# Kernel optimization log

Measured on AMD Instinct MI355X. Metric: run time of the kernel, lower is better.

The kernel has to match this reference:

```python
import jax, jax.numpy as jnp
import numpy as np
from jax import lax

DEPTH = 3
KS = 5

def haar_fwd(x):
    # x: (B, 2h, 2w, C) -> (B, h, w, C, 4) with bands [LL, LH, HL, HH]
    a = x[:, 0::2, 0::2]; b = x[:, 0::2, 1::2]
    c = x[:, 1::2, 0::2]; d = x[:, 1::2, 1::2]
    ll = (a + b + c + d) * 0.5
    lh = (a + b - c - d) * 0.5
    hl = (a - b + c - d) * 0.5
    hh = (a - b - c + d) * 0.5
    return jnp.stack([ll, lh, hl, hh], axis=-1)

def haar_inv(co):
    # co: (B, h, w, C, 4) -> (B, 2h, 2w, C); orthonormal inverse of haar_fwd
    ll, lh, hl, hh = co[..., 0], co[..., 1], co[..., 2], co[..., 3]
    a = (ll + lh + hl + hh) * 0.5
    b = (ll + lh - hl - hh) * 0.5
    c = (ll - lh + hl - hh) * 0.5
    d = (ll - lh - hl + hh) * 0.5
    B, h, w, C = ll.shape
    top = jnp.stack([a, b], axis=3).reshape(B, h, 2 * w, C)
    bot = jnp.stack([c, d], axis=3).reshape(B, h, 2 * w, C)
    return jnp.stack([top, bot], axis=2).reshape(B, 2 * h, 2 * w, C)

def depthwise(x, k, groups):
    return lax.conv_general_dilated(
        x, k, (1, 1), 'SAME',
        dimension_numbers=('NHWC', 'HWIO', 'NHWC'),
        feature_group_count=groups)

def setup_inputs() -> dict:
    key = jax.random.key(0)
    ks = jax.random.split(key, 2 + DEPTH)
    B, H, W, C = 8, 256, 256, 128
    x = jax.random.normal(ks[0], (B, H, W, C), jnp.float32)
    fan = float(KS * KS)
    base_kernel = jax.random.normal(ks[1], (KS, KS, 1, C), jnp.float32) / np.sqrt(fan)
    base_bias = jnp.zeros((C,), jnp.float32)
    base_scale = jnp.ones((1, 1, 1, C), jnp.float32)
    wavelet_kernels = tuple(
        jax.random.normal(ks[2 + i], (KS, KS, 1, C * 4), jnp.float32) / np.sqrt(fan)
        for i in range(DEPTH))
    wavelet_scales = tuple(jnp.full((1, 1, 1, C * 4), 0.1, jnp.float32) for _ in range(DEPTH))
    return dict(x=x, base_kernel=base_kernel, base_bias=base_bias, base_scale=base_scale,
                wavelet_kernels=wavelet_kernels, wavelet_scales=wavelet_scales)

def reference(x, base_kernel, base_bias, base_scale, wavelet_kernels, wavelet_scales):
    B, H, W, C = x.shape
    # pad input to even H/W (edge mode); no-op for even dims
    xp = jnp.pad(x, ((0, 0), (0, H % 2), (0, W % 2), (0, 0)), mode='edge')
    # multi-level Haar forward: level l decomposes the raw LL of level l-1
    coeffs, dims = [], []
    cur = xp
    for _ in range(DEPTH):
        _, h, w, _ = cur.shape
        dims.append((h, w))
        cur = jnp.pad(cur, ((0, 0), (0, h % 2), (0, w % 2), (0, 0)), mode='edge')
        co = haar_fwd(cur)
        coeffs.append(co)
        cur = co[..., 0]
    # per-level depthwise conv with scale fused into the kernel
    conv_coeffs = []
    for lvl in range(DEPTH):
        co = coeffs[lvl]
        Bc, h, w, Cc, _ = co.shape
        flat = co.reshape(Bc, h, w, Cc * 4)
        fused = wavelet_scales[lvl] * wavelet_kernels[lvl]  # (KS,KS,1,4C)
        out = depthwise(flat, fused, Cc * 4)
        conv_coeffs.append(out.reshape(Bc, h, w, Cc, 4))
    # inverse reconstruction with add of deeper reconstruction into LL band
    next_ll = jnp.zeros_like(conv_coeffs[-1][..., 0])
    for lvl in range(DEPTH - 1, -1, -1):
        co = conv_coeffs[lvl].at[..., 0].add(next_ll)
        rec = haar_inv(co)
        h, w = dims[lvl]
        next_ll = rec[:, :h, :w, :]
    output_wt = next_ll[:, :H, :W, :]
    x_base = base_scale * (depthwise(xp, base_kernel, C) + base_bias)[:, :H, :W, :]
    return x_base + output_wt
```

## Files before the change

### kernel.cpp

```cpp
#include <hip/hip_runtime.h>

#define NC 128
#define NB 8
#define CPB 32
#define R 2
#define JT 32

__device__ __forceinline__ float2 ld2(const float* p) { return *(const float2*)p; }
__device__ __forceinline__ float2 add2(float2 a, float2 b) { return make_float2(a.x + b.x, a.y + b.y); }
__device__ __forceinline__ float2 sub2(float2 a, float2 b) { return make_float2(a.x - b.x, a.y - b.y); }
__device__ __forceinline__ float2 muls2(float2 a, float s) { return make_float2(a.x * s, a.y * s); }
__device__ __forceinline__ float2 fma2(float2 a, float2 w, float2 c) {
    return make_float2(fmaf(a.x, w.x, c.x), fmaf(a.y, w.y, c.y));
}

__global__ __launch_bounds__(256) void k_haar_ll(
    const float* __restrict__ P, float* __restrict__ out, int h, int w)
{
    int idx = blockIdx.x * blockDim.x + threadIdx.x;
    int total = NB * h * w * (NC / 4);
    if (idx >= total) return;
    int cq = idx & (NC / 4 - 1);
    int t  = idx / (NC / 4);
    int j  = t % w; t /= w;
    int i  = t % h;
    int b  = t / h;
    size_t W2C  = (size_t)(2 * w) * NC;
    size_t base = (((size_t)b * (2 * h) + 2 * i) * (2 * w) + 2 * j) * NC + cq * 4;
    float4 A  = *(const float4*)(P + base);
    float4 Bv = *(const float4*)(P + base + NC);
    float4 Cv = *(const float4*)(P + base + W2C);
    float4 Dv = *(const float4*)(P + base + W2C + NC);
    float4 r;
    r.x = (A.x + Bv.x + Cv.x + Dv.x) * 0.5f;
    r.y = (A.y + Bv.y + Cv.y + Dv.y) * 0.5f;
    r.z = (A.z + Bv.z + Cv.z + Dv.z) * 0.5f;
    r.w = (A.w + Bv.w + Cv.w + Dv.w) * 0.5f;
    *(float4*)(out + (size_t)idx * 4) = r;
}

#define WL2(s, t)  (wl + ((s) * 25 + (t)) * CPB + 2 * tc)
#define WB2(m, n)  (wbase + ((m) * 5 + (n)) * CPB + 2 * tc)

template <bool BASE>
__global__ __launch_bounds__(256) void k_convinv(
    const float* __restrict__ P, const float* __restrict__ nll,
    const float* __restrict__ wk, const float* __restrict__ wsc,
    const float* __restrict__ bk, const float* __restrict__ bb,
    const float* __restrict__ bs, float* __restrict__ out,
    int h, int w)
{
    extern __shared__ float lds[];
    float* wl     = lds;
    float* wbase  = wl + 4 * 25 * CPB;
    float* bscale = wbase + 25 * CPB;
    float* bbias  = bscale + CPB;

    const int cg    = blockIdx.x & 3;
    const int jtile = blockIdx.x >> 2;
    const int c0    = cg * CPB;
    const int tid   = threadIdx.x + threadIdx.y * 16;

    for (int u = tid; u < 4 * 25 * CPB; u += 256) {
        int tcc = u & (CPB - 1);
        int st  = u / CPB;
        int t   = st % 25;
        int s   = st / 25;
        wl[u] = 0.5f * wsc[(c0 + tcc) * 4 + s] * wk[t * (4 * NC) + (c0 + tcc) * 4 + s];
    }
    if (BASE) {
        for (int u = tid; u < 25 * CPB; u += 256) {
            int tcc = u & (CPB - 1);
            int t   = u / CPB;
            wbase[u] = bk[t * NC + c0 + tcc];
        }
        if (tid < CPB) { bscale[tid] = bs[c0 + tid]; bbias[tid] = bb[c0 + tid]; }
    }
    __syncthreads();

    const int tc = threadIdx.x;
    const int cc = c0 + 2 * tc;
    const int b  = blockIdx.z;
    const int i  = blockIdx.y;
    const int ja = jtile * JT + threadIdx.y * R;
    const int PH = 2 * h;
    const size_t rowC = (size_t)(2 * w) * NC;

    int   coff[R + 4];
    float cmask[R + 4];
    #pragma unroll
    for (int q = 0; q < R + 4; ++q) {
        int xq  = ja + q - 2;
        int xqc = min(max(xq, 0), w - 1);
        coff[q]  = xqc * (2 * NC);
        cmask[q] = (xq >= 0 && xq < w) ? 1.f : 0.f;
    }

    float2 acc0[R], acc1[R], acc2[R], acc3[R];
    float2 bb00[R], bb01[R], bb10[R], bb11[R];
    #pragma unroll
    for (int s = 0; s < R; ++s) {
        acc0[s] = acc1[s] = acc2[s] = acc3[s] = make_float2(0.f, 0.f);
        bb00[s] = bb01[s] = bb10[s] = bb11[s] = make_float2(0.f, 0.f);
    }

    #pragma unroll
    for (int ky = 0; ky < 5; ++ky) {
        int y = i + ky - 2;
        if (y < 0 || y >= h) continue;

        const float* prA = P + ((size_t)b * PH + 2 * y) * rowC + cc;
        const float* prC = prA + rowC;
        #pragma unroll
        for (int q = 0; q < R + 4; ++q) {
            float m = cmask[q];
            const float* pA = prA + coff[q];
            const float* pC = prC + coff[q];
            float2 A  = muls2(ld2(pA), m);
            float2 Bv = muls2(ld2(pA + NC), m);
            float2 Cv = muls2(ld2(pC), m);
            float2 Dv = muls2(ld2(pC + NC), m);
            float2 sA = add2(A, Bv), sC = add2(Cv, Dv);
            float2 dA = sub2(A, Bv), dC = sub2(Cv, Dv);
            float2 s0 = add2(sA, sC), s1 = sub2(sA, sC);
            float2 s2 = add2(dA, dC), s3 = sub2(dA, dC);
            #pragma unroll
            for (int s = 0; s < R; ++s) {
                const int kx = q - s;
                if (kx < 0 || kx > 4) continue;
                const int t = ky * 5 + kx;
                acc0[s] = fma2(s0, ld2(WL2(0, t)), acc0[s]);
                acc1[s] = fma2(s1, ld2(WL2(1, t)), acc1[s]);
                acc2[s] = fma2(s2, ld2(WL2(2, t)), acc2[s]);
                acc3[s] = fma2(s3, ld2(WL2(3, t)), acc3[s]);
                if (BASE && ky >= 1 && ky <= 3 && kx >= 1 && kx <= 3) {
                    bb00[s] = fma2(A, ld2(WB2(2 * ky - 2, 2 * kx - 2)), bb00[s]);
                    if (kx >= 2)            bb01[s] = fma2(A,  ld2(WB2(2 * ky - 2, 2 * kx - 3)), bb01[s]);
                    if (ky >= 2)            bb10[s] = fma2(A,  ld2(WB2(2 * ky - 3, 2 * kx - 2)), bb10[s]);
                    if (ky >= 2 && kx >= 2) bb11[s] = fma2(A,  ld2(WB2(2 * ky - 3, 2 * kx - 3)), bb11[s]);
                    if (kx <= 2)            bb00[s] = fma2(Bv, ld2(WB2(2 * ky - 2, 2 * kx - 1)), bb00[s]);
                                            bb01[s] = fma2(Bv, ld2(WB2(2 * ky - 2, 2 * kx - 2)), bb01[s]);
                    if (ky >= 2 && kx <= 2) bb10[s] = fma2(Bv, ld2(WB2(2 * ky - 3, 2 * kx - 1)), bb10[s]);
                    if (ky >= 2)            bb11[s] = fma2(Bv, ld2(WB2(2 * ky - 3, 2 * kx - 2)), bb11[s]);
                    if (ky <= 2)            bb00[s] = fma2(Cv, ld2(WB2(2 * ky - 1, 2 * kx - 2)), bb00[s]);
                    if (ky <= 2 && kx >= 2) bb01[s] = fma2(Cv, ld2(WB2(2 * ky - 1, 2 * kx - 3)), bb01[s]);
                                            bb10[s] = fma2(Cv, ld2(WB2(2 * ky - 2, 2 * kx - 2)), bb10[s]);
                    if (kx >= 2)            bb11[s] = fma2(Cv, ld2(WB2(2 * ky - 2, 2 * kx - 3)), bb11[s]);
                    if (ky <= 2 && kx <= 2) bb00[s] = fma2(Dv, ld2(WB2(2 * ky - 1, 2 * kx - 1)), bb00[s]);
                    if (ky <= 2)            bb01[s] = fma2(Dv, ld2(WB2(2 * ky - 1, 2 * kx - 2)), bb01[s]);
                    if (kx <= 2)            bb10[s] = fma2(Dv, ld2(WB2(2 * ky - 2, 2 * kx - 1)), bb10[s]);
                                            bb11[s] = fma2(Dv, ld2(WB2(2 * ky - 2, 2 * kx - 2)), bb11[s]);
                }
            }
        }
    }

    #pragma unroll
    for (int s = 0; s < R; ++s) {
        int j = ja + s;
        float2 a0 = acc0[s];
        if (nll) a0 = add2(a0, ld2(nll + (((size_t)b * h + i) * w + j) * NC + cc));
        float2 av = muls2(add2(add2(a0, acc1[s]), add2(acc2[s], acc3[s])), 0.5f);
        float2 bv = muls2(sub2(add2(a0, acc1[s]), add2(acc2[s], acc3[s])), 0.5f);
        float2 cv = muls2(add2(sub2(a0, acc1[s]), sub2(acc2[s], acc3[s])), 0.5f);
        float2 dv = muls2(sub2(sub2(a0, acc1[s]), sub2(acc2[s], acc3[s])), 0.5f);

        size_t ob = ((size_t)b * PH + 2 * i) * rowC + (size_t)(2 * j) * NC + cc;
        if (BASE) {
            float2 sc = ld2(bscale + 2 * tc);
            float2 bi = ld2(bbias + 2 * tc);
            float2 o00 = add2(make_float2(sc.x * (bb00[s].x + bi.x), sc.y * (bb00[s].y + bi.y)), av);
            float2 o01 = add2(make_float2(sc.x * (bb01[s].x + bi.x), sc.y * (bb01[s].y + bi.y)), bv);
            float2 o10 = add2(make_float2(sc.x * (bb10[s].x + bi.x), sc.y * (bb10[s].y + bi.y)), cv);
            float2 o11 = add2(make_float2(sc.x * (bb11[s].x + bi.x), sc.y * (bb11[s].y + bi.y)), dv);
            *(float2*)(out + ob)             = o00;
            *(float2*)(out + ob + NC)        = o01;
            *(float2*)(out + ob + rowC)      = o10;
            *(float2*)(out + ob + rowC + NC) = o11;
        } else {
            *(float2*)(out + ob)             = av;
            *(float2*)(out + ob + NC)        = bv;
            *(float2*)(out + ob + rowC)      = cv;
            *(float2*)(out + ob + rowC + NC) = dv;
        }
    }
}

extern "C" void kernel_launch(void* const* d_in, const int* in_sizes, int n_in,
                              void* d_out, int out_size, void* d_ws, size_t ws_size,
                              hipStream_t stream)
{
    const float* x  = (const float*)d_in[0];
    const float* bk = (const float*)d_in[1];
    const float* bb = (const float*)d_in[2];
    const float* bs = (const float*)d_in[3];
    const float* wk[3];
    const float* wv[3];
    if (n_in >= 10) {
        for (int i = 0; i < 3; ++i) {
            wk[i] = (const float*)d_in[4 + i];
            wv[i] = (const float*)d_in[7 + i];
        }
    } else {
        const float* wkc = (const float*)d_in[4];
        const float* wvc = (const float*)d_in[5];
        for (int i = 0; i < 3; ++i) {
            wk[i] = wkc + (size_t)i * 25 * 4 * NC;
            wv[i] = wvc + (size_t)i * 4 * NC;
        }
    }
    float* out = (float*)d_out;

    float* ll0 = out;
    float* ll1 = out + 16777216;
    float* r2  = out + 16777216 + 4194304;
    float* r1  = (float*)d_ws;

    {
        int total = NB * 128 * 128 * (NC / 4);
        k_haar_ll<<<(total + 255) / 256, 256, 0, stream>>>(x, ll0, 128, 128);
    }
    {
        int total = NB * 64 * 64 * (NC / 4);
        k_haar_ll<<<(total + 255) / 256, 256, 0, stream>>>(ll0, ll1, 64, 64);
    }

    size_t lds_nb = (size_t)(4 * 25 * CPB) * sizeof(float);
    size_t lds_b  = (size_t)(4 * 25 * CPB + 25 * CPB + 2 * CPB) * sizeof(float);
    dim3 blk(16, 16);

    k_convinv<false><<<dim3((32 / JT) * 4, 32, NB), blk, lds_nb, stream>>>(
        ll1, nullptr, wk[2], wv[2], nullptr, nullptr, nullptr, r2, 32, 32);

    k_convinv<false><<<dim3((64 / JT) * 4, 64, NB), blk, lds_nb, stream>>>(
        ll0, r2, wk[1], wv[1], nullptr, nullptr, nullptr, r1, 64, 64);

    k_convinv<true><<<dim3((128 / JT) * 4, 128, NB), blk, lds_b, stream>>>(
        x, r1, wk[0], wv[0], bk, bb, bs, out, 128, 128);
}
```

Baseline: 646.3 us.

## Raise per-thread column blocking to 4 and split interior/boundary conv paths

Each thread now computes 4 output columns instead of 2, so it reuses more of the loaded input columns across outputs (R+4 loads for R outputs). The clamped-offset and mask arithmetic is dropped from an unmasked interior path, and edge threads take a separate per-output path with explicit bounds checks. Launch bounds now request 2 blocks per CU, and out-of-range threads return early for levels whose width is smaller than the tile. The cost is higher register pressure, since the BASE variant keeps 32 float2 accumulators, plus idle threads on the 32-wide level and divergence between interior and edge threads.

```diff
diff --git a/kernel.cpp b/kernel.cpp
--- a/kernel.cpp
+++ b/kernel.cpp
@@ -3,8 +3,8 @@
 #define NC 128
 #define NB 8
 #define CPB 32
-#define R 2
-#define JT 32
+#define R 4
+#define JT (16 * R)
 
 __device__ __forceinline__ float2 ld2(const float* p) { return *(const float2*)p; }
 __device__ __forceinline__ float2 add2(float2 a, float2 b) { return make_float2(a.x + b.x, a.y + b.y); }
@@ -43,7 +43,7 @@
 #define WB2(m, n)  (wbase + ((m) * 5 + (n)) * CPB + 2 * tc)
 
 template <bool BASE>
-__global__ __launch_bounds__(256) void k_convinv(
+__global__ __launch_bounds__(256, 2) void k_convinv(
     const float* __restrict__ P, const float* __restrict__ nll,
     const float* __restrict__ wk, const float* __restrict__ wsc,
     const float* __restrict__ bk, const float* __restrict__ bb,
@@ -83,18 +83,9 @@
     const int b  = blockIdx.z;
     const int i  = blockIdx.y;
     const int ja = jtile * JT + threadIdx.y * R;
+    if (ja >= w) return;
     const int PH = 2 * h;
     const size_t rowC = (size_t)(2 * w) * NC;
-
-    int   coff[R + 4];
-    float cmask[R + 4];
-    #pragma unroll
-    for (int q = 0; q < R + 4; ++q) {
-        int xq  = ja + q - 2;
-        int xqc = min(max(xq, 0), w - 1);
-        coff[q]  = xqc * (2 * NC);
-        cmask[q] = (xq >= 0 && xq < w) ? 1.f : 0.f;
-    }
 
     float2 acc0[R], acc1[R], acc2[R], acc3[R];
     float2 bb00[R], bb01[R], bb10[R], bb11[R];
@@ -104,52 +95,103 @@
         bb00[s] = bb01[s] = bb10[s] = bb11[s] = make_float2(0.f, 0.f);
     }
 
-    #pragma unroll
-    for (int ky = 0; ky < 5; ++ky) {
-        int y = i + ky - 2;
-        if (y < 0 || y >= h) continue;
-
-        const float* prA = P + ((size_t)b * PH + 2 * y) * rowC + cc;
-        const float* prC = prA + rowC;
+    const bool interior = (ja >= 2) && (ja <= w - R - 2);
+
+    if (interior) {
         #pragma unroll
-        for (int q = 0; q < R + 4; ++q) {
-            float m = cmask[q];
-            const float* pA = prA + coff[q];
-            const float* pC = prC + coff[q];
-            float2 A  = muls2(ld2(pA), m);
-            float2 Bv = muls2(ld2(pA + NC), m);
-            float2 Cv = muls2(ld2(pC), m);
-            float2 Dv = muls2(ld2(pC + NC), m);
-            float2 sA = add2(A, Bv), sC = add2(Cv, Dv);
-            float2 dA = sub2(A, Bv), dC = sub2(Cv, Dv);
-            float2 s0 = add2(sA, sC), s1 = sub2(sA, sC);
-            float2 s2 = add2(dA, dC), s3 = sub2(dA, dC);
+        for (int ky = 0; ky < 5; ++ky) {
+            int y = i + ky - 2;
+            if (y < 0 || y >= h) continue;
+
+            const float* pA0 = P + ((size_t)b * PH + 2 * y) * rowC
+                                 + (size_t)(ja - 2) * (2 * NC) + cc;
+            const float* pC0 = pA0 + rowC;
             #pragma unroll
-            for (int s = 0; s < R; ++s) {
-                const int kx = q - s;
-                if (kx < 0 || kx > 4) continue;
-                const int t = ky * 5 + kx;
-                acc0[s] = fma2(s0, ld2(WL2(0, t)), acc0[s]);
-                acc1[s] = fma2(s1, ld2(WL2(1, t)), acc1[s]);
-                acc2[s] = fma2(s2, ld2(WL2(2, t)), acc2[s]);
-                acc3[s] = fma2(s3, ld2(WL2(3, t)), acc3[s]);
-                if (BASE && ky >= 1 && ky <= 3 && kx >= 1 && kx <= 3) {
-                    bb00[s] = fma2(A, ld2(WB2(2 * ky - 2, 2 * kx - 2)), bb00[s]);
-                    if (kx >= 2)            bb01[s] = fma2(A,  ld2(WB2(2 * ky - 2, 2 * kx - 3)), bb01[s]);
-                    if (ky >= 2)            bb10[s] = fma2(A,  ld2(WB2(2 * ky - 3, 2 * kx - 2)), bb10[s]);
-                    if (ky >= 2 && kx >= 2) bb11[s] = fma2(A,  ld2(WB2(2 * ky - 3, 2 * kx - 3)), bb11[s]);
-                    if (kx <= 2)            bb00[s] = fma2(Bv, ld2(WB2(2 * ky - 2, 2 * kx - 1)), bb00[s]);
-                                            bb01[s] = fma2(Bv, ld2(WB2(2 * ky - 2, 2 * kx - 2)), bb01[s]);
-                    if (ky >= 2 && kx <= 2) bb10[s] = fma2(Bv, ld2(WB2(2 * ky - 3, 2 * kx - 1)), bb10[s]);
-                    if (ky >= 2)            bb11[s] = fma2(Bv, ld2(WB2(2 * ky - 3, 2 * kx - 2)), bb11[s]);
-                    if (ky <= 2)            bb00[s] = fma2(Cv, ld2(WB2(2 * ky - 1, 2 * kx - 2)), bb00[s]);
-                    if (ky <= 2 && kx >= 2) bb01[s] = fma2(Cv, ld2(WB2(2 * ky - 1, 2 * kx - 3)), bb01[s]);
-                                            bb10[s] = fma2(Cv, ld2(WB2(2 * ky - 2, 2 * kx - 2)), bb10[s]);
-                    if (kx >= 2)            bb11[s] = fma2(Cv, ld2(WB2(2 * ky - 2, 2 * kx - 3)), bb11[s]);
-                    if (ky <= 2 && kx <= 2) bb00[s] = fma2(Dv, ld2(WB2(2 * ky - 1, 2 * kx - 1)), bb00[s]);
-                    if (ky <= 2)            bb01[s] = fma2(Dv, ld2(WB2(2 * ky - 1, 2 * kx - 2)), bb01[s]);
-                    if (kx <= 2)            bb10[s] = fma2(Dv, ld2(WB2(2 * ky - 2, 2 * kx - 1)), bb10[s]);
-                                            bb11[s] = fma2(Dv, ld2(WB2(2 * ky - 2, 2 * kx - 2)), bb11[s]);
+            for (int q = 0; q < R + 4; ++q) {
+                float2 A  = ld2(pA0 + q * 2 * NC);
+                float2 Bv = ld2(pA0 + q * 2 * NC + NC);
+                float2 Cv = ld2(pC0 + q * 2 * NC);
+                float2 Dv = ld2(pC0 + q * 2 * NC + NC);
+                float2 sA = add2(A, Bv), sC = add2(Cv, Dv);
+                float2 dA = sub2(A, Bv), dC = sub2(Cv, Dv);
+                float2 s0 = add2(sA, sC), s1 = sub2(sA, sC);
+                float2 s2 = add2(dA, dC), s3 = sub2(dA, dC);
+                #pragma unroll
+                for (int s = 0; s < R; ++s) {
+                    const int kx = q - s;
+                    if (kx < 0 || kx > 4) continue;
+                    const int t = ky * 5 + kx;
+                    acc0[s] = fma2(s0, ld2(WL2(0, t)), acc0[s]);
+                    acc1[s] = fma2(s1, ld2(WL2(1, t)), acc1[s]);
+                    acc2[s] = fma2(s2, ld2(WL2(2, t)), acc2[s]);
+                    acc3[s] = fma2(s3, ld2(WL2(3, t)), acc3[s]);
+                    if (BASE && ky >= 1 && ky <= 3 && kx >= 1 && kx <= 3) {
+                        bb00[s] = fma2(A, ld2(WB2(2 * ky - 2, 2 * kx - 2)), bb00[s]);
+                        if (kx >= 2)            bb01[s] = fma2(A,  ld2(WB2(2 * ky - 2, 2 * kx - 3)), bb01[s]);
+                        if (ky >= 2)            bb10[s] = fma2(A,  ld2(WB2(2 * ky - 3, 2 * kx - 2)), bb10[s]);
+                        if (ky >= 2 && kx >= 2) bb11[s] = fma2(A,  ld2(WB2(2 * ky - 3, 2 * kx - 3)), bb11[s]);
+                        if (kx <= 2)            bb00[s] = fma2(Bv, ld2(WB2(2 * ky - 2, 2 * kx - 1)), bb00[s]);
+                                                bb01[s] = fma2(Bv, ld2(WB2(2 * ky - 2, 2 * kx - 2)), bb01[s]);
+                        if (ky >= 2 && kx <= 2) bb10[s] = fma2(Bv, ld2(WB2(2 * ky - 3, 2 * kx - 1)), bb10[s]);
+                        if (ky >= 2)            bb11[s] = fma2(Bv, ld2(WB2(2 * ky - 3, 2 * kx - 2)), bb11[s]);
+                        if (ky <= 2)            bb00[s] = fma2(Cv, ld2(WB2(2 * ky - 1, 2 * kx - 2)), bb00[s]);
+                        if (ky <= 2 && kx >= 2) bb01[s] = fma2(Cv, ld2(WB2(2 * ky - 1, 2 * kx - 3)), bb01[s]);
+                                                bb10[s] = fma2(Cv, ld2(WB2(2 * ky - 2, 2 * kx - 2)), bb10[s]);
+                        if (kx >= 2)            bb11[s] = fma2(Cv, ld2(WB2(2 * ky - 2, 2 * kx - 3)), bb11[s]);
+                        if (ky <= 2 && kx <= 2) bb00[s] = fma2(Dv, ld2(WB2(2 * ky - 1, 2 * kx - 1)), bb00[s]);
+                        if (ky <= 2)            bb01[s] = fma2(Dv, ld2(WB2(2 * ky - 1, 2 * kx - 2)), bb01[s]);
+                        if (kx <= 2)            bb10[s] = fma2(Dv, ld2(WB2(2 * ky - 2, 2 * kx - 1)), bb10[s]);
+                                                bb11[s] = fma2(Dv, ld2(WB2(2 * ky - 2, 2 * kx - 2)), bb11[s]);
+                    }
+                }
+            }
+        }
+    } else {
+        #pragma unroll
+        for (int s = 0; s < R; ++s) {
+            int j = ja + s;
+            if (j >= w) break;
+            #pragma unroll
+            for (int ky = 0; ky < 5; ++ky) {
+                int y = i + ky - 2;
+                if (y < 0 || y >= h) continue;
+                const float* prA = P + ((size_t)b * PH + 2 * y) * rowC + cc;
+                const float* prC = prA + rowC;
+                #pragma unroll
+                for (int kx = 0; kx < 5; ++kx) {
+                    int xq = j + kx - 2;
+                    if (xq < 0 || xq >= w) continue;
+                    const float* pA = prA + (size_t)xq * (2 * NC);
+                    const float* pC = prC + (size_t)xq * (2 * NC);
+                    float2 A  = ld2(pA);
+                    float2 Bv = ld2(pA + NC);
+                    float2 Cv = ld2(pC);
+                    float2 Dv = ld2(pC + NC);
+                    float2 sA = add2(A, Bv), sC = add2(Cv, Dv);
+                    float2 dA = sub2(A, Bv), dC = sub2(Cv, Dv);
+                    const int t = ky * 5 + kx;
+                    acc0[s] = fma2(add2(sA, sC), ld2(WL2(0, t)), acc0[s]);
+                    acc1[s] = fma2(sub2(sA, sC), ld2(WL2(1, t)), acc1[s]);
+                    acc2[s] = fma2(add2(dA, dC), ld2(WL2(2, t)), acc2[s]);
+                    acc3[s] = fma2(sub2(dA, dC), ld2(WL2(3, t)), acc3[s]);
+                    if (BASE && ky >= 1 && ky <= 3 && kx >= 1 && kx <= 3) {
+                        bb00[s] = fma2(A, ld2(WB2(2 * ky - 2, 2 * kx - 2)), bb00[s]);
+                        if (kx >= 2)            bb01[s] = fma2(A,  ld2(WB2(2 * ky - 2, 2 * kx - 3)), bb01[s]);
+                        if (ky >= 2)            bb10[s] = fma2(A,  ld2(WB2(2 * ky - 3, 2 * kx - 2)), bb10[s]);
+                        if (ky >= 2 && kx >= 2) bb11[s] = fma2(A,  ld2(WB2(2 * ky - 3, 2 * kx - 3)), bb11[s]);
+                        if (kx <= 2)            bb00[s] = fma2(Bv, ld2(WB2(2 * ky - 2, 2 * kx - 1)), bb00[s]);
+                                                bb01[s] = fma2(Bv, ld2(WB2(2 * ky - 2, 2 * kx - 2)), bb01[s]);
+                        if (ky >= 2 && kx <= 2) bb10[s] = fma2(Bv, ld2(WB2(2 * ky - 3, 2 * kx - 1)), bb10[s]);
+                        if (ky >= 2)            bb11[s] = fma2(Bv, ld2(WB2(2 * ky - 3, 2 * kx - 2)), bb11[s]);
+                        if (ky <= 2)            bb00[s] = fma2(Cv, ld2(WB2(2 * ky - 1, 2 * kx - 2)), bb00[s]);
+                        if (ky <= 2 && kx >= 2) bb01[s] = fma2(Cv, ld2(WB2(2 * ky - 1, 2 * kx - 3)), bb01[s]);
+                                                bb10[s] = fma2(Cv, ld2(WB2(2 * ky - 2, 2 * kx - 2)), bb10[s]);
+                        if (kx >= 2)            bb11[s] = fma2(Cv, ld2(WB2(2 * ky - 2, 2 * kx - 3)), bb11[s]);
+                        if (ky <= 2 && kx <= 2) bb00[s] = fma2(Dv, ld2(WB2(2 * ky - 1, 2 * kx - 1)), bb00[s]);
+                        if (ky <= 2)            bb01[s] = fma2(Dv, ld2(WB2(2 * ky - 1, 2 * kx - 2)), bb01[s]);
+                        if (kx <= 2)            bb10[s] = fma2(Dv, ld2(WB2(2 * ky - 2, 2 * kx - 1)), bb10[s]);
+                                                bb11[s] = fma2(Dv, ld2(WB2(2 * ky - 2, 2 * kx - 2)), bb11[s]);
+                    }
                 }
             }
         }
@@ -158,6 +200,7 @@
     #pragma unroll
     for (int s = 0; s < R; ++s) {
         int j = ja + s;
+        if (j >= w) break;
         float2 a0 = acc0[s];
         if (nll) a0 = add2(a0, ld2(nll + (((size_t)b * h + i) * w + j) * NC + cc));
         float2 av = muls2(add2(add2(a0, acc1[s]), add2(acc2[s], acc3[s])), 0.5f);
@@ -169,14 +212,10 @@
         if (BASE) {
             float2 sc = ld2(bscale + 2 * tc);
             float2 bi = ld2(bbias + 2 * tc);
-            float2 o00 = add2(make_float2(sc.x * (bb00[s].x + bi.x), sc.y * (bb00[s].y + bi.y)), av);
-            float2 o01 = add2(make_float2(sc.x * (bb01[s].x + bi.x), sc.y * (bb01[s].y + bi.y)), bv);
-            float2 o10 = add2(make_float2(sc.x * (bb10[s].x + bi.x), sc.y * (bb10[s].y + bi.y)), cv);
-            float2 o11 = add2(make_float2(sc.x * (bb11[s].x + bi.x), sc.y * (bb11[s].y + bi.y)), dv);
-            *(float2*)(out + ob)             = o00;
-            *(float2*)(out + ob + NC)        = o01;
-            *(float2*)(out + ob + rowC)      = o10;
-            *(float2*)(out + ob + rowC + NC) = o11;
+            *(float2*)(out + ob)             = add2(make_float2(sc.x * (bb00[s].x + bi.x), sc.y * (bb00[s].y + bi.y)), av);
+            *(float2*)(out + ob + NC)        = add2(make_float2(sc.x * (bb01[s].x + bi.x), sc.y * (bb01[s].y + bi.y)), bv);
+            *(float2*)(out + ob + rowC)      = add2(make_float2(sc.x * (bb10[s].x + bi.x), sc.y * (bb10[s].y + bi.y)), cv);
+            *(float2*)(out + ob + rowC + NC) = add2(make_float2(sc.x * (bb11[s].x + bi.x), sc.y * (bb11[s].y + bi.y)), dv);
         } else {
             *(float2*)(out + ob)             = av;
             *(float2*)(out + ob + NC)        = bv;
@@ -229,12 +268,12 @@
     size_t lds_b  = (size_t)(4 * 25 * CPB + 25 * CPB + 2 * CPB) * sizeof(float);
     dim3 blk(16, 16);
 
-    k_convinv<false><<<dim3((32 / JT) * 4, 32, NB), blk, lds_nb, stream>>>(
+    k_convinv<false><<<dim3(((32 + JT - 1) / JT) * 4, 32, NB), blk, lds_nb, stream>>>(
         ll1, nullptr, wk[2], wv[2], nullptr, nullptr, nullptr, r2, 32, 32);
 
-    k_convinv<false><<<dim3((64 / JT) * 4, 64, NB), blk, lds_nb, stream>>>(
+    k_convinv<false><<<dim3(((64 + JT - 1) / JT) * 4, 64, NB), blk, lds_nb, stream>>>(
         ll0, r2, wk[1], wv[1], nullptr, nullptr, nullptr, r1, 64, 64);
 
-    k_convinv<true><<<dim3((128 / JT) * 4, 128, NB), blk, lds_b, stream>>>(
+    k_convinv<true><<<dim3(((128 + JT - 1) / JT) * 4, 128, NB), blk, lds_b, stream>>>(
         x, r1, wk[0], wv[0], bk, bb, bs, out, 128, 128);
 }
```

Result: slower. 710.3 us (+9.9%).
